# Optimization experiments

Measured on AMD Instinct MI355X. Metric: run time of the kernel, lower is better.

## Reference

```python
import math
import jax, jax.numpy as jnp
import numpy as np

B, HRV, WRV, CRV = 1, 32, 512, 64
CBEV, HB, WB = 128, 256, 256
D, COUT, K, HEADS, P = 128, 128, 5, 8, 6
HD = D // HEADS
NBINS = 110
RMAX, BIN = 55.0, 0.5
XMIN, XMAX, YMIN, YMAX = -55.0, 55.0, -55.0, 55.0

_ELEV = np.array([-30.67, -29.33, -28.0, -26.66, -25.33, -24.0, -22.67, -21.33,
                  -20.0, -18.67, -17.33, -16.0, -14.67, -13.33, -12.0, -10.67,
                  -9.33, -8.0, -6.66, -5.33, -4.0, -2.67, -1.33, 0.0, 1.33,
                  2.67, 4.0, 5.33, 6.67, 8.0, 9.33, 10.67], dtype=np.float32)

def _make_uvec():
    az_line = np.linspace(-math.pi, math.pi, WRV + 1, dtype=np.float32)[:-1]
    az = az_line + 0.5 * (az_line[1] - az_line[0])
    elev = np.deg2rad(_ELEV[::-1].reshape(HRV, -1).mean(axis=1)).astype(np.float32)
    az2 = np.broadcast_to(az[None, :], (HRV, WRV))
    el2 = np.broadcast_to(elev[:, None], (HRV, WRV))
    ux = np.cos(az2) * np.cos(el2)
    uy = np.sin(az2) * np.cos(el2)
    uz = np.broadcast_to(np.sin(el2), (HRV, WRV))
    return jnp.asarray(ux), jnp.asarray(uy), jnp.asarray(uz)

_UX, _UY, _UZ = _make_uvec()

def _lin(x, w, b):
    # 1x1 conv / Linear: w is torch-layout [Cout, Cin]
    return jnp.einsum('...c,oc->...o', x, w) + b

def _gn(x, gamma, beta, groups, eps=1e-5):
    Bn, H, W, C = x.shape
    xg = x.reshape(Bn, H, W, groups, C // groups)
    mu = xg.mean(axis=(1, 2, 4), keepdims=True)
    var = ((xg - mu) ** 2).mean(axis=(1, 2, 4), keepdims=True)
    xg = (xg - mu) * jax.lax.rsqrt(var + eps)
    return xg.reshape(Bn, H, W, C) * gamma + beta

def _gelu(x):
    return jax.nn.gelu(x, approximate=False)

def _conv3x3_circ(x, w):
    # torch Conv2d(3x3, padding=1, padding_mode='circular', bias=False)
    xp = jnp.pad(x, ((0, 0), (1, 1), (1, 1), (0, 0)), mode='wrap')
    k = jnp.transpose(w, (2, 3, 1, 0))  # OIHW -> HWIO
    return jax.lax.conv_general_dilated(xp, k, (1, 1), 'VALID',
                                        dimension_numbers=('NHWC', 'HWIO', 'NHWC'))

def _deform_sample(v, loc, aw):
    # v: [B, HB*WB, HEADS, HD]; loc: [B,Nq,HEADS,P,2] normalized; aw: [B,Nq,HEADS,P]
    # Emulates grid_sample(bilinear, zeros padding, align_corners=False).
    Bq = v.shape[0]
    vflat = jnp.transpose(v, (0, 2, 1, 3))       # [B, H, HW, hd]
    loc_t = jnp.transpose(loc, (0, 2, 1, 3, 4))  # [B, H, Nq, P, 2]
    aw_t = jnp.transpose(aw, (0, 2, 1, 3))       # [B, H, Nq, P]
    x = loc_t[..., 0] * WB - 0.5
    y = loc_t[..., 1] * HB - 0.5
    x0 = jnp.floor(x); y0 = jnp.floor(y)
    wx1 = x - x0; wy1 = y - y0
    x0i = x0.astype(jnp.int32); y0i = y0.astype(jnp.int32)
    gather = jax.vmap(jax.vmap(lambda vf, idx: vf[idx]))  # over B, heads
    def corner(xi, yi, wgt, acc):
        valid = (xi >= 0) & (xi < WB) & (yi >= 0) & (yi < HB)
        idx = jnp.clip(yi, 0, HB - 1) * WB + jnp.clip(xi, 0, WB - 1)
        g = gather(vflat, idx)  # [B, H, Nq, P, hd]
        return acc + g * (wgt * valid.astype(g.dtype))[..., None]
    acc = jnp.zeros(x.shape + (HD,), dtype=v.dtype)
    acc = corner(x0i,     y0i,     (1 - wx1) * (1 - wy1), acc)
    acc = corner(x0i + 1, y0i,     wx1 * (1 - wy1), acc)
    acc = corner(x0i,     y0i + 1, (1 - wx1) * wy1, acc)
    acc = corner(x0i + 1, y0i + 1, wx1 * wy1, acc)
    out = (acc * aw_t[..., None]).sum(axis=3)    # [B, H, Nq, hd]
    return jnp.transpose(out, (0, 2, 1, 3)).reshape(Bq, -1, D)

def _forward(x_rv, bev, lidar2ego_mat, wq, bq, wv, bv, wo, bo,
             qd_w1, qd_b1, qd_w2, qd_b2,
             rh_w1, rh_b1, rh_g1, rh_be1, rh_w2, rh_g2, rh_be2, rh_w3, rh_b3,
             off_w, off_b, aw_w, aw_b, vp_w, vp_b, op_w, op_b):
    Bq = x_rv.shape[0]
    Q0 = _lin(x_rv, wq, bq)                                   # [B,Hrv,Wrv,D]
    Vmap = _lin(jnp.transpose(bev, (0, 2, 3, 1)), wv, bv)     # [B,HB,WB,D]
    uvec = jnp.broadcast_to(jnp.stack([_UX, _UY, _UZ], axis=-1)[None], (Bq, HRV, WRV, 3))
    h = _gelu(_gn(_lin(jnp.concatenate([x_rv, uvec], axis=-1), rh_w1, rh_b1), rh_g1, rh_be1, 8))
    h = _gelu(_gn(_conv3x3_circ(h, rh_w2), rh_g2, rh_be2, 8))
    depth_logits = _lin(h, rh_w3, rh_b3)                      # [B,Hrv,Wrv,NBINS]
    depth_dist = jax.nn.softmax(depth_logits, axis=-1)
    topk_prob, topk_idx = jax.lax.top_k(depth_dist, K)        # [B,Hrv,Wrv,K]
    topk_depths = jnp.minimum(BIN * (topk_idx.astype(jnp.float32) + 0.5), RMAX - 0.5 * BIN)
    xl = topk_depths * _UX[None, :, :, None]
    yl = topk_depths * _UY[None, :, :, None]
    zl = topk_depths * _UZ[None, :, :, None]
    p = jnp.stack([xl, yl, zl, jnp.ones_like(xl)], axis=-1)   # [B,Hrv,Wrv,K,4]
    pe = jnp.einsum('bhwki,ij->bhwkj', p, lidar2ego_mat[0])
    rx = (pe[..., 0] - XMIN) / (XMAX - XMIN)
    ry = (pe[..., 1] - YMIN) / (YMAX - YMIN)
    ref_pts = jnp.stack([jnp.clip(rx, 0.0, 1.0), jnp.clip(ry, 0.0, 1.0)], axis=-1).reshape(Bq, -1, 2)
    qin = jnp.concatenate([jnp.broadcast_to(Q0[:, :, :, None, :], (Bq, HRV, WRV, K, D)),
                           (topk_depths / RMAX)[..., None]], axis=-1)
    query = _lin(_gelu(_lin(qin, qd_w1, qd_b1)), qd_w2, qd_b2).reshape(Bq, -1, D)
    value = Vmap.reshape(Bq, -1, D)
    # --- MSDA (mmcv MultiScaleDeformableAttention, 1 level) ---
    v = _lin(value, vp_w, vp_b).reshape(Bq, -1, HEADS, HD)
    Nq = query.shape[1]
    off = _lin(query, off_w, off_b).reshape(Bq, Nq, HEADS, P, 2)
    aw = jax.nn.softmax(_lin(query, aw_w, aw_b).reshape(Bq, Nq, HEADS, P), axis=-1)
    loc = ref_pts[:, :, None, None, :] + off / jnp.array([WB, HB], dtype=jnp.float32)
    y_msda = _lin(_deform_sample(v, loc, aw), op_w, op_b) + query  # residual add
    y_msda = y_msda.reshape(Bq, HRV, WRV, K, D)
    wgt = topk_prob / (topk_prob.sum(axis=-1, keepdims=True) + 1e-8)
    y = (y_msda * wgt[..., None]).sum(axis=3)
    y = _lin(y, wo, bo)                                       # [B,Hrv,Wrv,COUT]
    return y, jnp.transpose(depth_logits, (0, 3, 1, 2))

def setup_inputs():
    key = jax.random.key(0)
    ks = jax.random.split(key, 32)
    def rn(i, shape, s):
        return jax.random.normal(ks[i], shape, dtype=jnp.float32) * s
    return dict(
        x_rv=rn(0, (B, HRV, WRV, CRV), 1.0),
        bev=rn(1, (B, CBEV, HB, WB), 1.0),
        lidar2ego_mat=jnp.eye(4, dtype=jnp.float32)[None] + rn(2, (1, 4, 4), 0.01),
        wq=rn(3, (D, CRV), 0.05), bq=rn(4, (D,), 0.01),
        wv=rn(5, (D, CBEV), 0.05), bv=rn(6, (D,), 0.01),
        wo=rn(7, (COUT, D), 0.05), bo=rn(8, (COUT,), 0.01),
        qd_w1=rn(9, (D, D + 1), 0.05), qd_b1=rn(10, (D,), 0.01),
        qd_w2=rn(11, (D, D), 0.05), qd_b2=rn(12, (D,), 0.01),
        rh_w1=rn(13, (128, CRV + 3), 0.05), rh_b1=rn(14, (128,), 0.01),
        rh_g1=jnp.ones((128,), jnp.float32), rh_be1=jnp.zeros((128,), jnp.float32),
        rh_w2=rn(15, (64, 128, 3, 3), 0.05),
        rh_g2=jnp.ones((64,), jnp.float32), rh_be2=jnp.zeros((64,), jnp.float32),
        rh_w3=rn(16, (NBINS, 64), 0.05), rh_b3=rn(17, (NBINS,), 0.01),
        off_w=rn(18, (HEADS * P * 2, D), 0.02), off_b=rn(19, (HEADS * P * 2,), 2.0),
        aw_w=rn(20, (HEADS * P, D), 0.02), aw_b=rn(21, (HEADS * P,), 0.01),
        vp_w=rn(22, (D, D), 0.05), vp_b=rn(23, (D,), 0.01),
        op_w=rn(24, (D, D), 0.05), op_b=rn(25, (D,), 0.01),
    )

def reference(x_rv, bev, lidar2ego_mat, wq, bq, wv, bv, wo, bo,
              qd_w1, qd_b1, qd_w2, qd_b2,
              rh_w1, rh_b1, rh_g1, rh_be1, rh_w2, rh_g2, rh_be2, rh_w3, rh_b3,
              off_w, off_b, aw_w, aw_b, vp_w, vp_b, op_w, op_b):
    return _forward(x_rv, bev, lidar2ego_mat, wq, bq, wv, bv, wo, bo,
                    qd_w1, qd_b1, qd_w2, qd_b2,
                    rh_w1, rh_b1, rh_g1, rh_be1, rh_w2, rh_g2, rh_be2, rh_w3, rh_b3,
                    off_w, off_b, aw_w, aw_b, vp_w, vp_b, op_w, op_b)
```

## Files before the change

kernel.cpp:

```cpp
#include <hip/hip_runtime.h>
#include <math.h>

#define NT 256

typedef unsigned short u16;
typedef unsigned int u32;
typedef _Float16 f16;
typedef __attribute__((ext_vector_type(2))) unsigned int u32x2;
typedef __attribute__((ext_vector_type(4))) unsigned int u32x4;
typedef __attribute__((ext_vector_type(4))) float f32x4;
typedef __attribute__((ext_vector_type(8))) short s16x8;
typedef __attribute__((ext_vector_type(8))) _Float16 f16x8;

namespace {

__device__ const float c_elev[32] = {
  -30.67f,-29.33f,-28.0f,-26.66f,-25.33f,-24.0f,-22.67f,-21.33f,
  -20.0f,-18.67f,-17.33f,-16.0f,-14.67f,-13.33f,-12.0f,-10.67f,
  -9.33f,-8.0f,-6.66f,-5.33f,-4.0f,-2.67f,-1.33f,0.0f,1.33f,
  2.67f,4.0f,5.33f,6.67f,8.0f,9.33f,10.67f };

__device__ __forceinline__ float gelu_f(float x) {
  return 0.5f * x * (1.0f + erff(x * 0.70710678118654752440f));
}
// ... 15 lines not shown
__device__ __forceinline__ u32 packsplit(float x) {
  f16 h = (f16)x;
  f16 l = (f16)(x - (float)h);
  return (u32)__builtin_bit_cast(u16, h) | ((u32)__builtin_bit_cast(u16, l) << 16);
}
__device__ __forceinline__ void unpack16(u32x4 a, u32x4 b, f16x8& hi, f16x8& lo) {
  u32x4 h, l;
  h[0] = (a[0] & 0xFFFFu) | (a[1] << 16);  l[0] = (a[0] >> 16) | (a[1] & 0xFFFF0000u);
  h[1] = (a[2] & 0xFFFFu) | (a[3] << 16);  l[1] = (a[2] >> 16) | (a[3] & 0xFFFF0000u);
  h[2] = (b[0] & 0xFFFFu) | (b[1] << 16);  l[2] = (b[0] >> 16) | (b[1] & 0xFFFF0000u);
  h[3] = (b[2] & 0xFFFFu) | (b[3] << 16);  l[3] = (b[2] >> 16) | (b[3] & 0xFFFF0000u);
  hi = __builtin_bit_cast(f16x8, h);
  lo = __builtin_bit_cast(f16x8, l);
}

template<int COREAL, int CO, int KPAD, int CI, int PROD, int AMODE, bool DOGELU, bool OBF>
__global__ __launch_bounds__(NT)
void slin(const float* __restrict__ Af, const float* __restrict__ A2,
          const u32* __restrict__ Wp, const float* __restrict__ bias,
          float* __restrict__ outF, u16* __restrict__ outB)
{
  constexpr int BM = 64;
  constexpr int NFR = CO / 16;
  constexpr int KS = KPAD / 32;
  __shared__ u32 lds[BM * KPAD];
  const int tid = threadIdx.x;
  const long row0 = (long)blockIdx.x * BM;

  for (int i = tid; i < BM * (KPAD / 4); i += NT) {
    int r = i / (KPAD / 4), c = (i % (KPAD / 4)) * 4;
    long pix = row0 + r;
    u32x4 o;
    if constexpr (AMODE == 0) {
      if (c + 3 < CI) {
        f32x4 v = *(const f32x4*)(Af + pix * CI + c);
#pragma unroll
        for (int e = 0; e < 4; e++) o[e] = packsplit(v[e]);
      } else {
#pragma unroll
        for (int e = 0; e < 4; e++) {
          int cc = c + e;
          o[e] = packsplit(cc < CI ? Af[pix * CI + cc] : 0.f);
        }
      }
    } else {
      if (c + 3 < 64) {
        f32x4 v = *(const f32x4*)(Af + pix * 64 + c);
#pragma unroll
        for (int e = 0; e < 4; e++) o[e] = packsplit(v[e]);
      } else {
#pragma unroll
        for (int e = 0; e < 4; e++) {
          int cc = c + e;
          float x = (cc < 64) ? Af[pix * 64 + cc] : ((cc < 67) ? A2[pix * 3 + cc - 64] : 0.f);
          o[e] = packsplit(x);
        }
      }
// ... 37 lines not shown
    if (col >= COREAL) continue;
    float bcol = bias[col];
#pragma unroll
    for (int r = 0; r < 4; r++) {
      long row = row0 + mb + kq * 4 + r;
      float val = acc[nf][r] + bcol;
      if constexpr (DOGELU) val = gelu_f(val);
      if constexpr (OBF) outB[row * COREAL + col] = bf16rne(val);
      else               outF[row * COREAL + col] = val;
    }
  }
}

__global__ __launch_bounds__(NT)
void conv_mfma(const float* __restrict__ X, const u32* __restrict__ Wc,
               float* __restrict__ Y)
{
  __shared__ u32 lds[4 * 18 * 128];
  const int tid = threadIdx.x;
  const int bRow = (blockIdx.x >> 5) * 2;
  const int bCol = (blockIdx.x & 31) * 16;

  for (int i = tid; i < 4 * 18 * 32; i += NT) {
    int c4 = (i & 31) * 4;
    int col = (i >> 5) % 18;
    int row = i / (18 * 32);
    int gy = (bRow + row - 1 + 32) & 31;
    int gx = (bCol + col - 1 + 512) & 511;
    f32x4 v = *(const f32x4*)(X + ((long)gy * 512 + gx) * 128 + c4);
    u32x4 o;
#pragma unroll
    for (int e = 0; e < 4; e++) o[e] = packsplit(v[e]);
    *(u32x4*)((char*)lds + ((((row * 18 + col) * 128 + c4) * 4) ^ ((col & 7) << 4))) = o;
  }
  __syncthreads();

  const int wave = tid >> 6, lane = tid & 63;
  const int wm = wave >> 1;
  const int nb = (wave & 1) * 32;
  const int lr = lane & 15, kq = lane >> 4;

  f32x4 acc[2] = {};
  for (int t = 0; t < 9; t++) {
    const int ky = t / 3, kx = t % 3;
    const int wrow = wm + ky;
    const int wcol = lr + kx;
    const u32 sw = (wcol & 7) << 4;
// ... 120 lines not shown
        if constexpr (DEPTH) val += ew * (A2[row] * (1.0f / 55.0f));
        if constexpr (DOGELU) val = gelu_f(val);
        if constexpr (SPLIT) {
          if (col < 96) outF[row * 96 + col] = val;
          else if (col < 144) outB[row * 48 + (col - 96)] = bf16rne(val);
        } else {
          if constexpr (WF) outF[row * CO + col] = val;
          if constexpr (WBF) outB[row * CO + col] = bf16rne(val);
        }
      }
    }
  }
}

__global__ __launch_bounds__(NT)
void final_gemm(const u16* __restrict__ A, const u16* __restrict__ Wc,
                const float* __restrict__ cvec, float* __restrict__ outY)
{
  __shared__ char As[64 * 512];
  const int tid = threadIdx.x;
  const long row0 = (long)blockIdx.x * 64;
  for (int i = tid; i < 64 * 32; i += NT) {
    int r = i >> 5, ck = i & 31;
    u32x4 v = ((const u32x4*)(A + (row0 + r) * 256))[ck];
    *(u32x4*)(As + ((r * 512 + ck * 16) ^ ((r & 7) << 4))) = v;
  }
  __syncthreads();
  const int wave = tid >> 6, lane = tid & 63;
  const int mb = wave * 16;
  const int lr = lane & 15, kq = lane >> 4;
  f32x4 acc[8] = {};
#pragma unroll
  for (int ks = 0; ks < 8; ks++) {
    const int kof = (ks * 32 + kq * 8) * 2;
    const int r = mb + lr;
    s16x8 af = *(const s16x8*)(As + ((r * 512 + kof) ^ ((r & 7) << 4)));
#pragma unroll
    for (int nf = 0; nf < 8; nf++) {
      s16x8 bfr = *(const s16x8*)(Wc + (nf * 16 + lr) * 256 + ks * 32 + kq * 8);
      acc[nf] = __builtin_amdgcn_mfma_f32_16x16x32_bf16(af, bfr, acc[nf], 0, 0, 0);
    }
  }
#pragma unroll
  for (int nf = 0; nf < 8; nf++) {
    int col = nf * 16 + lr;
    float bcol = cvec[col];
#pragma unroll
    for (int r = 0; r < 4; r++) {
      long row = row0 + mb + kq * 4 + r;
      outY[row * 128 + col] = acc[nf][r] + bcol;
    }
  }
}

__global__ __launch_bounds__(NT)
void combine_kernel(const u16* __restrict__ smp, const u16* __restrict__ query,
                    const float* __restrict__ wgt, u16* __restrict__ acat)
{
  const long idx = (long)blockIdx.x * NT + threadIdx.x;
  const long pix = idx >> 3;
  const int c0 = (idx & 7) * 16;
  float w[5];
#pragma unroll
  for (int k = 0; k < 5; k++) w[k] = wgt[pix * 5 + k];
  float as[16] = {}, aq[16] = {};
#pragma unroll
  for (int k = 0; k < 5; k++) {
    const u32x4* sp = (const u32x4*)(smp + (pix * 5 + k) * 128 + c0);
    const u32x4* qp = (const u32x4*)(query + (pix * 5 + k) * 128 + c0);
    u32x4 s0 = sp[0], s1 = sp[1], q0 = qp[0], q1 = qp[1];
#pragma unroll
    for (int e = 0; e < 4; e++) {
      as[2 * e]     += w[k] * bflo(s0[e]);  as[2 * e + 1] += w[k] * bfhi(s0[e]);
      as[8 + 2 * e] += w[k] * bflo(s1[e]);  as[9 + 2 * e] += w[k] * bfhi(s1[e]);
      aq[2 * e]     += w[k] * bflo(q0[e]);  aq[2 * e + 1] += w[k] * bfhi(q0[e]);
      aq[8 + 2 * e] += w[k] * bflo(q1[e]);  aq[9 + 2 * e] += w[k] * bfhi(q1[e]);
    }
  }
  u32x4 o0, o1, o2, o3;
#pragma unroll
  for (int e = 0; e < 4; e++) {
    o0[e] = (u32)bf16rne(as[2 * e]) | ((u32)bf16rne(as[2 * e + 1]) << 16);
    o1[e] = (u32)bf16rne(as[8 + 2 * e]) | ((u32)bf16rne(as[9 + 2 * e]) << 16);
    o2[e] = (u32)bf16rne(aq[2 * e]) | ((u32)bf16rne(aq[2 * e + 1]) << 16);
    o3[e] = (u32)bf16rne(aq[8 + 2 * e]) | ((u32)bf16rne(aq[9 + 2 * e]) << 16);
  }
  u32x4* dst = (u32x4*)(acat + pix * 256 + c0);
  dst[0] = o0; dst[1] = o1;
  u32x4* dst2 = (u32x4*)(acat + pix * 256 + 128 + c0);
  dst2[0] = o2; dst2[1] = o3;
}

__global__ void wcomb_kernel(const float* __restrict__ vp_w, const float* __restrict__ wv,
                             const float* __restrict__ vp_b, const float* __restrict__ bv,
                             u16* __restrict__ wc, float* __restrict__ bc)
{
  int o = blockIdx.x;
  int c = threadIdx.x;
  float s = 0.f;
  for (int m = 0; m < 128; m++) s += vp_w[o * 128 + m] * wv[m * 128 + c];
  wc[o * 128 + c] = bf16rne(s);
  if (c == 0) {
    float b = vp_b[o];
    for (int m = 0; m < 128; m++) b += vp_w[o * 128 + m] * bv[m];
    bc[o] = b;
  }
}

__global__ void wopcomb_kernel(const float* __restrict__ wo, const float* __restrict__ op_w,
                               const float* __restrict__ op_b, const float* __restrict__ bo,
                               u16* __restrict__ Wcat, float* __restrict__ cvec)
{
  int o = blockIdx.x;
  int c = threadIdx.x;
  float s = 0.f;
  for (int m = 0; m < 128; m++) s += wo[o * 128 + m] * op_w[m * 128 + c];
  Wcat[o * 256 + c] = bf16rne(s);
  Wcat[o * 256 + 128 + c] = bf16rne(wo[o * 128 + c]);
  if (c == 0) {
    float b = bo[o];
    for (int m = 0; m < 128; m++) b += wo[o * 128 + m] * op_b[m];
    cvec[o] = b;
  }
}

__global__ void cvtw_kernel(const float* __restrict__ qd_w1, const float* __restrict__ qd_w2,
                            const float* __restrict__ off_w, const float* __restrict__ aw_w,
                            const float* __restrict__ off_b, const float* __restrict__ aw_b,
                            u16* Wq1, u16* Wq2, u16* Wmg, float* mgbias, float* w1last)
{
  int i = blockIdx.x * NT + threadIdx.x;
  if (i < 16384) {
    int r = i >> 7, c = i & 127;
    Wq1[i] = bf16rne(qd_w1[r * 129 + c]);
    Wq2[i] = bf16rne(qd_w2[i]);
  }
  if (i < 20480) {
    int r = i >> 7, c = i & 127;
    float v = (r < 96) ? off_w[r * 128 + c] : ((r < 144) ? aw_w[(r - 96) * 128 + c] : 0.f);
    Wmg[i] = bf16rne(v);
  }
  if (i < 160) mgbias[i] = (i < 96) ? off_b[i] : ((i < 144) ? aw_b[i - 96] : 0.f);
  if (i < 128) w1last[i] = qd_w1[i * 129 + 128];
}

__global__ void packw_kernel(const float* __restrict__ rh_w1, const float* __restrict__ rh_w3,
                             const float* __restrict__ wq, const float* __restrict__ rh_w2,
                             u32* Wh1, u32* Wlog, u32* Wq0, u32* Wcv)
{
  int i = blockIdx.x * NT + threadIdx.x;
  if (i < 128 * 96) {
    int r = i / 96, c = i % 96;
    Wh1[i] = packsplit(c < 67 ? rh_w1[r * 67 + c] : 0.f);
  }
  if (i < 112 * 64) {
    int r = i / 64, c = i % 64;
    Wlog[i] = packsplit(r < 110 ? rh_w3[r * 64 + c] : 0.f);
  }
  if (i < 128 * 64) Wq0[i] = packsplit(wq[i]);
  if (i < 9 * 64 * 128) {
    int t = i / (64 * 128), o = (i / 128) % 64, c = i % 128;
    Wcv[i] = packsplit(rh_w2[(o * 128 + c) * 9 + t]);
  }
}

__global__ void uvec_kernel(float* __restrict__ uvec)
{
  int pix = blockIdx.x * NT + threadIdx.x;
  if (pix >= 16384) return;
  int hr = pix >> 9;
  int w = pix & 511;
  float el = c_elev[31 - hr] * 0.017453292519943295f;
  float az = -3.14159265358979323846f + ((float)w + 0.5f) * (6.283185307179586477f / 512.0f);
  float ce = cosf(el);
  uvec[pix * 3 + 0] = cosf(az) * ce;
  uvec[pix * 3 + 1] = sinf(az) * ce;
  uvec[pix * 3 + 2] = sinf(el);
}

template<int C, int S>
__global__ __launch_bounds__(NT)
void gn_stats_kernel(const float* __restrict__ X, int Npix, float* __restrict__ gs)
{
  constexpr int PPB = NT / C;
  int tid = threadIdx.x;
  int c = tid % C;
  int psub = tid / C;
  float sum = 0.f, ss = 0.f;
  for (long pix = (long)blockIdx.x * PPB + psub; pix < Npix; pix += (long)gridDim.x * PPB) {
    float v = X[pix * C + c];
    sum += v; ss += v * v;
  }
  __shared__ float ls[8][2];
  if (tid < 16) ls[tid / 2][tid % 2] = 0.f;
  __syncthreads();
  int g = c / S;
  atomicAdd(&ls[g][0], sum);
  atomicAdd(&ls[g][1], ss);
  __syncthreads();
  if (tid < 16) atomicAdd(&gs[tid], ls[tid / 2][tid % 2]);
}

template<int C, int S>
__global__ void gn_apply_kernel(float* __restrict__ X, long total, int Npix,
                                const float* __restrict__ gs,
                                const float* __restrict__ gamma, const float* __restrict__ beta)
{
  float cnt = (float)Npix * (float)S;
  for (long i = (long)blockIdx.x * NT + threadIdx.x; i < total; i += (long)gridDim.x * NT) {
    int c = (int)(i % C);
    int g = c / S;
    float mu = gs[g * 2] / cnt;
    float var = gs[g * 2 + 1] / cnt - mu * mu;
    float v = (X[i] - mu) * rsqrtf(var + 1e-5f);
    v = v * gamma[c] + beta[c];
    X[i] = gelu_f(v);
  }
}

__global__ __launch_bounds__(NT)
void tlogits_kernel(const float* __restrict__ logits, float* __restrict__ out1)
{
  __shared__ float ls[128][111];
  int p0 = blockIdx.x * 128;
  for (int i = threadIdx.x; i < 128 * 110; i += NT) {
    int p = i / 110, c = i % 110;
    ls[p][c] = logits[(long)(p0 + p) * 110 + c];
  }
  __syncthreads();
  for (int i = threadIdx.x; i < 110 * 128; i += NT) {
    int c = i / 128, p = i % 128;
    out1[(long)c * 16384 + p0 + p] = ls[p][c];
  }
}
// ... 27 lines not shown
    pr[j] = expf(bv - m) / den;
    pi[j] = bi;
    if (bi == lane) v0 = -1e30f;
    if (bi == lane + 64) v1 = -1e30f;
  }
  if (lane == 0) {
    float tot = pr[0] + pr[1] + pr[2] + pr[3] + pr[4] + 1e-8f;
#pragma unroll
    for (int j = 0; j < 5; j++) {
      depths[pix * 5 + j] = fminf(0.5f * ((float)pi[j] + 0.5f), 54.75f);
      wgt[pix * 5 + j] = pr[j] / tot;
    }
  }
}

__global__ void refq_kernel(const float* __restrict__ depths, const float* __restrict__ uvec,
                            const float* __restrict__ L44, float* __restrict__ refq)
{
  long q = (long)blockIdx.x * NT + threadIdx.x;
  if (q >= 81920) return;
  long pix = q / 5;
  float d = depths[q];
  float px = d * uvec[pix * 3 + 0];
  float py = d * uvec[pix * 3 + 1];
  float pz = d * uvec[pix * 3 + 2];
  float pex = px * L44[0] + py * L44[4] + pz * L44[8] + L44[12];
  float pey = px * L44[1] + py * L44[5] + pz * L44[9] + L44[13];
  float rx = (pex + 55.0f) / 110.0f;
  float ry = (pey + 55.0f) / 110.0f;
  refq[q * 2 + 0] = fminf(fmaxf(rx, 0.f), 1.f);
  refq[q * 2 + 1] = fminf(fmaxf(ry, 0.f), 1.f);
}

__global__ __launch_bounds__(NT)
void msda_kernel(const u16* __restrict__ V, const float* __restrict__ refq,
                 const float* __restrict__ offb, const u16* __restrict__ awb,
                 u16* __restrict__ S)
{
  const int tid = threadIdx.x;
  const int kk = blockIdx.x >> 9;
  const int pg = blockIdx.x & 511;
  const long pix = (long)pg * 32 + (tid >> 3);
  const int h = tid & 7;
  const long q = pix * 5 + kk;
  const int c0 = h * 16;
  const float rx = refq[q * 2 + 0], ry = refq[q * 2 + 1];

  const u32* ap32 = (const u32*)(awb + q * 48 + h * 6);
  u32 aw0 = ap32[0], aw1 = ap32[1], aw2 = ap32[2];
  float a[6] = { bflo(aw0), bfhi(aw0), bflo(aw1), bfhi(aw1), bflo(aw2), bfhi(aw2) };
  float mx = fmaxf(fmaxf(fmaxf(a[0], a[1]), fmaxf(a[2], a[3])), fmaxf(a[4], a[5]));
  float se = 0.f;
#pragma unroll
  for (int p = 0; p < 6; p++) { a[p] = __expf(a[p] - mx); se += a[p]; }
  const float inv = 1.0f / se;

  const f32x4* opv = (const f32x4*)(offb + q * 96 + h * 12);
  f32x4 of0 = opv[0], of1 = opv[1], of2 = opv[2];
  const float ox[6] = { of0[0], of0[2], of1[0], of1[2], of2[0], of2[2] };
  const float oy[6] = { of0[1], of0[3], of1[1], of1[3], of2[1], of2[3] };

  float acc[16];
#pragma unroll
  for (int j = 0; j < 16; j++) acc[j] = 0.f;

#pragma unroll
  for (int p = 0; p < 6; p++) {
    float x = (rx + ox[p] * (1.0f / 256.0f)) * 256.0f - 0.5f;
    float y = (ry + oy[p] * (1.0f / 256.0f)) * 256.0f - 0.5f;
    float x0f = floorf(x), y0f = floorf(y);
    float wx = x - x0f, wy = y - y0f;
    int ix = (int)x0f, iy = (int)y0f;
    float awp = a[p] * inv;
    float wx0 = ((unsigned)ix < 256u) ? (1.f - wx) : 0.f;
    float wx1 = ((unsigned)(ix + 1) < 256u) ? wx : 0.f;
    float wy0 = ((unsigned)iy < 256u) ? (awp * (1.f - wy)) : 0.f;
    float wy1 = ((unsigned)(iy + 1) < 256u) ? (awp * wy) : 0.f;
    int xc0 = min(max(ix, 0), 255), xc1 = min(max(ix + 1, 0), 255);
    int yc0 = min(max(iy, 0), 255), yc1 = min(max(iy + 1, 0), 255);
#pragma unroll
    for (int cy = 0; cy < 2; cy++) {
      int yc = cy ? yc1 : yc0;
      float wyv = cy ? wy1 : wy0;
#pragma unroll
      for (int cx = 0; cx < 2; cx++) {
        int xc = cx ? xc1 : xc0;
        float m = (cx ? wx1 : wx0) * wyv;
        const u32x4* vp = (const u32x4*)(V + (yc * 256 + xc) * 128 + c0);
        u32x4 v0 = vp[0], v1 = vp[1];
#pragma unroll
        for (int e = 0; e < 4; e++) {
          acc[2 * e]     += m * bflo(v0[e]);  acc[2 * e + 1] += m * bfhi(v0[e]);
          acc[8 + 2 * e] += m * bflo(v1[e]);  acc[9 + 2 * e] += m * bfhi(v1[e]);
        }
      }
    }
  }
  u32x4 o0, o1;
#pragma unroll
  for (int e = 0; e < 4; e++) {
    o0[e] = (u32)bf16rne(acc[2 * e]) | ((u32)bf16rne(acc[2 * e + 1]) << 16);
    o1[e] = (u32)bf16rne(acc[8 + 2 * e]) | ((u32)bf16rne(acc[9 + 2 * e]) << 16);
  }
  u32x4* dst = (u32x4*)(S + q * 128 + c0);
  dst[0] = o0; dst[1] = o1;
}

}

extern "C" void kernel_launch(void* const* d_in, const int* in_sizes, int n_in,
                              void* d_out, int out_size, void* d_ws, size_t ws_size,
                              hipStream_t stream)
{
  (void)in_sizes; (void)n_in; (void)out_size; (void)ws_size;
  const float* x_rv   = (const float*)d_in[0];
  const float* bev    = (const float*)d_in[1];
  const float* L44    = (const float*)d_in[2];
  const float* wq     = (const float*)d_in[3];
  const float* bq     = (const float*)d_in[4];
  const float* wv     = (const float*)d_in[5];
// ... 27 lines not shown

  char* wsb = (char*)d_ws;
  size_t off = 0;
  auto alloc = [&](size_t bytes) -> char* {
    char* p = wsb + off;
    off += (bytes + 255) & ~(size_t)255;
    return p;
  };

  u16*   wcomb  = (u16*)alloc(32768);
  float* bcomb  = (float*)alloc(512);
  float* uvec   = (float*)alloc(196608);
  float* stats  = (float*)alloc(128);
  float* depths = (float*)alloc(327680);
  float* wgtb   = (float*)alloc(327680);
  float* refqb  = (float*)alloc(655360);
  float* w1last = (float*)alloc(512);
  u16*   Wq1    = (u16*)alloc(32768);
  u16*   Wq2    = (u16*)alloc(32768);
  u16*   Wmg    = (u16*)alloc(40960);
  float* mgbias = (float*)alloc(640);
  u16*   Wcat   = (u16*)alloc(65536);
  float* cvec   = (float*)alloc(512);
  u32*   Wh1    = (u32*)alloc(49152);
  u32*   Wlog   = (u32*)alloc(28672);
  u32*   Wq0    = (u32*)alloc(32768);
  u32*   Wcv    = (u32*)alloc(294912);
  char*  S1     = alloc(20971520);
  char*  S2     = alloc(4194304);
  char*  S3     = alloc(16777216);
  char*  S4     = alloc(20971520);
  char*  S5     = alloc(20971520);
  float* offbuf = (float*)alloc(31457280);
  u16*   awbf   = (u16*)alloc(7864320);

  float* h1buf  = (float*)S1;
  float* logits = (float*)(S1 + 8388608);
  float* h2buf  = (float*)(S1 + 15597568);
  u16*   smp    = (u16*)S1;
  u16*   Q0bf   = (u16*)S2;
  u16*   vbuf   = (u16*)S3;
  u16*   q1bf   = (u16*)S4;
  u16*   acat   = (u16*)S4;
  u16*   querybf= (u16*)S5;

  float* stats1 = stats;
  float* stats2 = stats + 16;

  hipMemsetAsync((void*)stats, 0, 128, stream);

  wcomb_kernel<<<128, 128, 0, stream>>>(vp_w, wv, vp_b, bv, wcomb, bcomb);
  wopcomb_kernel<<<128, 128, 0, stream>>>(woW, op_w, op_b, boB, Wcat, cvec);
  uvec_kernel<<<64, NT, 0, stream>>>(uvec);
  cvtw_kernel<<<80, NT, 0, stream>>>(qd_w1, qd_w2, off_w, aw_w, off_b, aw_b,
                                     Wq1, Wq2, Wmg, mgbias, w1last);
  packw_kernel<<<288, NT, 0, stream>>>(rh_w1, rh_w3, wq, rh_w2, Wh1, Wlog, Wq0, Wcv);

  slin<128, 128, 64, 64, 1, 0, false, true><<<256, NT, 0, stream>>>(
      x_rv, nullptr, Wq0, bq, nullptr, Q0bf);

  slin<128, 128, 96, 67, 3, 1, false, false><<<256, NT, 0, stream>>>(
      x_rv, uvec, Wh1, rh_b1, h1buf, nullptr);
  gn_stats_kernel<128, 16><<<512, NT, 0, stream>>>(h1buf, 16384, stats1);
  gn_apply_kernel<128, 16><<<2048, NT, 0, stream>>>(h1buf, 16384L * 128, 16384, stats1, rh_g1, rh_be1);
  conv_mfma<<<512, NT, 0, stream>>>(h1buf, Wcv, h2buf);
  gn_stats_kernel<64, 8><<<512, NT, 0, stream>>>(h2buf, 16384, stats2);
  gn_apply_kernel<64, 8><<<1024, NT, 0, stream>>>(h2buf, 16384L * 64, 16384, stats2, rh_g2, rh_be2);
  slin<110, 112, 64, 64, 3, 0, false, false><<<256, NT, 0, stream>>>(
      h2buf, nullptr, Wlog, rh_b3, logits, nullptr);
  tlogits_kernel<<<128, NT, 0, stream>>>(logits, outL);
  topk_kernel<<<4096, NT, 0, stream>>>(logits, depths, wgtb);
  refq_kernel<<<320, NT, 0, stream>>>(depths, uvec, L44, refqb);

  mfma_lin<128, 4, false, false, false, true, false><<<1024, NT, 0, stream>>>(
      bev, nullptr, wcomb, bcomb, nullptr, nullptr, vbuf, 65536);

  mfma_lin<128, 1, true, true, false, true, false><<<1280, NT, 0, stream>>>(
      Q0bf, depths, Wq1, qd_b1, w1last, nullptr, q1bf, 0);
  mfma_lin<128, 0, false, false, false, true, false><<<1280, NT, 0, stream>>>(
      q1bf, nullptr, Wq2, qd_b2, nullptr, nullptr, querybf, 0);

  mfma_lin<160, 0, false, false, false, false, true><<<1280, NT, 0, stream>>>(
      querybf, nullptr, Wmg, mgbias, nullptr, offbuf, awbf, 0);

  msda_kernel<<<2560, NT, 0, stream>>>(vbuf, refqb, offbuf, awbf, smp);

  combine_kernel<<<512, NT, 0, stream>>>(smp, querybf, wgtb, acat);

  final_gemm<<<256, NT, 0, stream>>>(acat, Wcat, cvec, outY);
}
```

Measured before the change: 452.3 us.

## Fuse GroupNorm apply, query MLP, combine/outproj, refq, and merge prep kernels

New measurement: 406.9 us. -10.0%, faster.

```diff
diff --git a/kernel.cpp b/kernel.cpp
--- a/kernel.cpp
+++ b/kernel.cpp
@@ -53,10 +53,12 @@
   lo = __builtin_bit_cast(f16x8, l);
 }
 
-template<int COREAL, int CO, int KPAD, int CI, int PROD, int AMODE, bool DOGELU, bool OBF>
+template<int COREAL, int CO, int KPAD, int CI, int PROD, int AMODE, bool DOGELU, bool OBF, bool GN = false>
 __global__ __launch_bounds__(NT)
 void slin(const float* __restrict__ Af, const float* __restrict__ A2,
           const u32* __restrict__ Wp, const float* __restrict__ bias,
+          const float* __restrict__ gs, const float* __restrict__ gamma,
+          const float* __restrict__ beta,
           float* __restrict__ outF, u16* __restrict__ outB)
 {
   constexpr int BM = 64;
@@ -74,12 +76,32 @@
       if (c + 3 < CI) {
         f32x4 v = *(const f32x4*)(Af + pix * CI + c);
 #pragma unroll
-        for (int e = 0; e < 4; e++) o[e] = packsplit(v[e]);
+        for (int e = 0; e < 4; e++) {
+          float x = v[e];
+          if constexpr (GN) {
+            int cc = c + e, g = cc >> 3;
+            float mu = gs[2 * g] * (1.0f / 131072.0f);
+            float var = gs[2 * g + 1] * (1.0f / 131072.0f) - mu * mu;
+            x = (x - mu) * rsqrtf(var + 1e-5f) * gamma[cc] + beta[cc];
+            x = gelu_f(x);
+          }
+          o[e] = packsplit(x);
+        }
       } else {
 #pragma unroll
         for (int e = 0; e < 4; e++) {
           int cc = c + e;
-          o[e] = packsplit(cc < CI ? Af[pix * CI + cc] : 0.f);
+          float x = (cc < CI) ? Af[pix * CI + cc] : 0.f;
+          if constexpr (GN) {
+            if (cc < CI) {
+              int g = cc >> 3;
+              float mu = gs[2 * g] * (1.0f / 131072.0f);
+              float var = gs[2 * g + 1] * (1.0f / 131072.0f) - mu * mu;
+              x = (x - mu) * rsqrtf(var + 1e-5f) * gamma[cc] + beta[cc];
+              x = gelu_f(x);
+            }
+          }
+          o[e] = packsplit(x);
         }
       }
     } else {
@@ -147,7 +169,8 @@
 
 __global__ __launch_bounds__(NT)
 void conv_mfma(const float* __restrict__ X, const u32* __restrict__ Wc,
-               float* __restrict__ Y)
+               const float* __restrict__ gs, const float* __restrict__ gamma,
+               const float* __restrict__ beta, float* __restrict__ Y)
 {
   __shared__ u32 lds[4 * 18 * 128];
   const int tid = threadIdx.x;
@@ -163,7 +186,13 @@
     f32x4 v = *(const f32x4*)(X + ((long)gy * 512 + gx) * 128 + c4);
     u32x4 o;
 #pragma unroll
-    for (int e = 0; e < 4; e++) o[e] = packsplit(v[e]);
+    for (int e = 0; e < 4; e++) {
+      int cc = c4 + e, g = cc >> 4;
+      float mu = gs[2 * g] * (1.0f / 262144.0f);
+      float var = gs[2 * g + 1] * (1.0f / 262144.0f) - mu * mu;
+      float x = (v[e] - mu) * rsqrtf(var + 1e-5f) * gamma[cc] + beta[cc];
+      o[e] = packsplit(gelu_f(x));
+    }
     *(u32x4*)((char*)lds + ((((row * 18 + col) * 128 + c4) * 4) ^ ((col & 7) << 4))) = o;
   }
   __syncthreads();
@@ -314,120 +343,230 @@
 }
 
 __global__ __launch_bounds__(NT)
-void final_gemm(const u16* __restrict__ A, const u16* __restrict__ Wc,
-                const float* __restrict__ cvec, float* __restrict__ outY)
+void qmlp_kernel(const u16* __restrict__ Q0, const float* __restrict__ depths,
+                 const u16* __restrict__ W1, const float* __restrict__ b1,
+                 const float* __restrict__ w1last,
+                 const u16* __restrict__ W2, const float* __restrict__ b2,
+                 u16* __restrict__ query)
+{
+  __shared__ char smem[49152];
+  char* As = smem;
+  char* Bs = smem + 16384;
+  const int tid = threadIdx.x;
+  const long row0 = (long)blockIdx.x * 64;
+
+  for (int i = tid; i < 128 * 16; i += NT) {
+    int r = i >> 4, ck = i & 15;
+    u32x4 v = ((const u32x4*)(W1 + r * 128))[ck];
+    *(u32x4*)(Bs + ((r * 256 + ck * 16) ^ ((r & 7) << 4))) = v;
+  }
+  for (int i = tid; i < 64 * 16; i += NT) {
+    int r = i >> 4, ck = i & 15;
+    long src = (row0 + r) / 5;
+    u32x4 v = ((const u32x4*)(Q0 + src * 128))[ck];
+    *(u32x4*)(As + ((r * 256 + ck * 16) ^ ((r & 7) << 4))) = v;
+  }
+  __syncthreads();
+
+  const int wave = tid >> 6, lane = tid & 63;
+  const int wm = wave >> 1, wn = wave & 1;
+  const int mb = wm * 32, nb = wn * 64;
+  const int lr = lane & 15, kq = lane >> 4;
+
+  f32x4 acc[2][4] = {};
+#pragma unroll
+  for (int ks = 0; ks < 4; ks++) {
+    const int kof = (ks * 32 + kq * 8) * 2;
+    s16x8 af[2], bfr[4];
+#pragma unroll
+    for (int mf = 0; mf < 2; mf++) {
+      int r = mb + mf * 16 + lr;
+      af[mf] = *(const s16x8*)(As + ((r * 256 + kof) ^ ((r & 7) << 4)));
+    }
+#pragma unroll
+    for (int nf = 0; nf < 4; nf++) {
+      int r = nb + nf * 16 + lr;
+      bfr[nf] = *(const s16x8*)(Bs + ((r * 256 + kof) ^ ((r & 7) << 4)));
+    }
+#pragma unroll
+    for (int mf = 0; mf < 2; mf++)
+#pragma unroll
+      for (int nf = 0; nf < 4; nf++)
+        acc[mf][nf] = __builtin_amdgcn_mfma_f32_16x16x32_bf16(af[mf], bfr[nf], acc[mf][nf], 0, 0, 0);
+  }
+  __syncthreads();
+
+#pragma unroll
+  for (int mf = 0; mf < 2; mf++) {
+#pragma unroll
+    for (int nf = 0; nf < 4; nf++) {
+      int col = nb + nf * 16 + lr;
+      float bcol = b1[col], ew = w1last[col];
+#pragma unroll
+      for (int r = 0; r < 4; r++) {
+        int lrow = mb + mf * 16 + kq * 4 + r;
+        float val = acc[mf][nf][r] + bcol + ew * (depths[row0 + lrow] * (1.0f / 55.0f));
+        val = gelu_f(val);
+        *(u16*)(As + ((lrow * 256 + col * 2) ^ ((lrow & 7) << 4))) = bf16rne(val);
+      }
+    }
+  }
+  for (int i = tid; i < 128 * 16; i += NT) {
+    int r = i >> 4, ck = i & 15;
+    u32x4 v = ((const u32x4*)(W2 + r * 128))[ck];
+    *(u32x4*)(Bs + ((r * 256 + ck * 16) ^ ((r & 7) << 4))) = v;
+  }
+  __syncthreads();
+
+  f32x4 acc2[2][4] = {};
+#pragma unroll
+  for (int ks = 0; ks < 4; ks++) {
+    const int kof = (ks * 32 + kq * 8) * 2;
+    s16x8 af[2], bfr[4];
+#pragma unroll
+    for (int mf = 0; mf < 2; mf++) {
+      int r = mb + mf * 16 + lr;
+      af[mf] = *(const s16x8*)(As + ((r * 256 + kof) ^ ((r & 7) << 4)));
+    }
+#pragma unroll
+    for (int nf = 0; nf < 4; nf++) {
+      int r = nb + nf * 16 + lr;
+      bfr[nf] = *(const s16x8*)(Bs + ((r * 256 + kof) ^ ((r & 7) << 4)));
+    }
+#pragma unroll
+    for (int mf = 0; mf < 2; mf++)
+#pragma unroll
+      for (int nf = 0; nf < 4; nf++)
+        acc2[mf][nf] = __builtin_amdgcn_mfma_f32_16x16x32_bf16(af[mf], bfr[nf], acc2[mf][nf], 0, 0, 0);
+  }
+#pragma unroll
+  for (int mf = 0; mf < 2; mf++) {
+#pragma unroll
+    for (int nf = 0; nf < 4; nf++) {
+      int col = nb + nf * 16 + lr;
+      float bcol = b2[col];
+#pragma unroll
+      for (int r = 0; r < 4; r++) {
+        long row = row0 + mb + mf * 16 + kq * 4 + r;
+        query[row * 128 + col] = bf16rne(acc2[mf][nf][r] + bcol);
+      }
+    }
+  }
+}
+
+__global__ __launch_bounds__(NT)
+void outproj_kernel(const u16* __restrict__ smp, const u16* __restrict__ query,
+                    const float* __restrict__ wgt, const u16* __restrict__ Wcat,
+                    const float* __restrict__ cvec, float* __restrict__ outY)
 {
   __shared__ char As[64 * 512];
   const int tid = threadIdx.x;
-  const long row0 = (long)blockIdx.x * 64;
-  for (int i = tid; i < 64 * 32; i += NT) {
-    int r = i >> 5, ck = i & 31;
-    u32x4 v = ((const u32x4*)(A + (row0 + r) * 256))[ck];
-    *(u32x4*)(As + ((r * 512 + ck * 16) ^ ((r & 7) << 4))) = v;
-  }
-  __syncthreads();
+  const long pix0 = (long)blockIdx.x * 64;
+
+#pragma unroll
+  for (int t = 0; t < 8; t++) {
+    int task = tid + t * 256;
+    int r = task >> 5, ch = task & 31;
+    long pix = pix0 + r;
+    const u16* src = (ch < 16) ? smp : query;
+    int cc = (ch & 15) * 8;
+    float acc[8] = {};
+#pragma unroll
+    for (int k = 0; k < 5; k++) {
+      float w = wgt[pix * 5 + k];
+      u32x4 v = *(const u32x4*)(src + (pix * 5 + k) * 128 + cc);
+#pragma unroll
+      for (int e = 0; e < 4; e++) {
+        acc[2 * e]     += w * bflo(v[e]);
+        acc[2 * e + 1] += w * bfhi(v[e]);
+      }
+    }
+    u32x4 o;
+#pragma unroll
+    for (int e = 0; e < 4; e++)
+      o[e] = (u32)bf16rne(acc[2 * e]) | ((u32)bf16rne(acc[2 * e + 1]) << 16);
+    *(u32x4*)(As + ((r * 512 + ch * 16) ^ ((r & 7) << 4))) = o;
+  }
+  __syncthreads();
+
   const int wave = tid >> 6, lane = tid & 63;
-  const int mb = wave * 16;
+  const int wm = wave >> 1, wn = wave & 1;
+  const int mb = wm * 32, nb = wn * 64;
   const int lr = lane & 15, kq = lane >> 4;
-  f32x4 acc[8] = {};
+
+  f32x4 acc[2][4] = {};
 #pragma unroll
   for (int ks = 0; ks < 8; ks++) {
     const int kof = (ks * 32 + kq * 8) * 2;
-    const int r = mb + lr;
-    s16x8 af = *(const s16x8*)(As + ((r * 512 + kof) ^ ((r & 7) << 4)));
-#pragma unroll
-    for (int nf = 0; nf < 8; nf++) {
-      s16x8 bfr = *(const s16x8*)(Wc + (nf * 16 + lr) * 256 + ks * 32 + kq * 8);
-      acc[nf] = __builtin_amdgcn_mfma_f32_16x16x32_bf16(af, bfr, acc[nf], 0, 0, 0);
-    }
-  }
-#pragma unroll
-  for (int nf = 0; nf < 8; nf++) {
-    int col = nf * 16 + lr;
-    float bcol = cvec[col];
-#pragma unroll
-    for (int r = 0; r < 4; r++) {
-      long row = row0 + mb + kq * 4 + r;
-      outY[row * 128 + col] = acc[nf][r] + bcol;
-    }
-  }
-}
-
-__global__ __launch_bounds__(NT)
-void combine_kernel(const u16* __restrict__ smp, const u16* __restrict__ query,
-                    const float* __restrict__ wgt, u16* __restrict__ acat)
-{
-  const long idx = (long)blockIdx.x * NT + threadIdx.x;
-  const long pix = idx >> 3;
-  const int c0 = (idx & 7) * 16;
-  float w[5];
-#pragma unroll
-  for (int k = 0; k < 5; k++) w[k] = wgt[pix * 5 + k];
-  float as[16] = {}, aq[16] = {};
-#pragma unroll
-  for (int k = 0; k < 5; k++) {
-    const u32x4* sp = (const u32x4*)(smp + (pix * 5 + k) * 128 + c0);
-    const u32x4* qp = (const u32x4*)(query + (pix * 5 + k) * 128 + c0);
-    u32x4 s0 = sp[0], s1 = sp[1], q0 = qp[0], q1 = qp[1];
-#pragma unroll
-    for (int e = 0; e < 4; e++) {
-      as[2 * e]     += w[k] * bflo(s0[e]);  as[2 * e + 1] += w[k] * bfhi(s0[e]);
-      as[8 + 2 * e] += w[k] * bflo(s1[e]);  as[9 + 2 * e] += w[k] * bfhi(s1[e]);
-      aq[2 * e]     += w[k] * bflo(q0[e]);  aq[2 * e + 1] += w[k] * bfhi(q0[e]);
-      aq[8 + 2 * e] += w[k] * bflo(q1[e]);  aq[9 + 2 * e] += w[k] * bfhi(q1[e]);
-    }
-  }
-  u32x4 o0, o1, o2, o3;
-#pragma unroll
-  for (int e = 0; e < 4; e++) {
-    o0[e] = (u32)bf16rne(as[2 * e]) | ((u32)bf16rne(as[2 * e + 1]) << 16);
-    o1[e] = (u32)bf16rne(as[8 + 2 * e]) | ((u32)bf16rne(as[9 + 2 * e]) << 16);
-    o2[e] = (u32)bf16rne(aq[2 * e]) | ((u32)bf16rne(aq[2 * e + 1]) << 16);
-    o3[e] = (u32)bf16rne(aq[8 + 2 * e]) | ((u32)bf16rne(aq[9 + 2 * e]) << 16);
-  }
-  u32x4* dst = (u32x4*)(acat + pix * 256 + c0);
-  dst[0] = o0; dst[1] = o1;
-  u32x4* dst2 = (u32x4*)(acat + pix * 256 + 128 + c0);
-  dst2[0] = o2; dst2[1] = o3;
-}
-
-__global__ void wcomb_kernel(const float* __restrict__ vp_w, const float* __restrict__ wv,
-                             const float* __restrict__ vp_b, const float* __restrict__ bv,
-                             u16* __restrict__ wc, float* __restrict__ bc)
-{
-  int o = blockIdx.x;
-  int c = threadIdx.x;
-  float s = 0.f;
-  for (int m = 0; m < 128; m++) s += vp_w[o * 128 + m] * wv[m * 128 + c];
-  wc[o * 128 + c] = bf16rne(s);
-  if (c == 0) {
-    float b = vp_b[o];
-    for (int m = 0; m < 128; m++) b += vp_w[o * 128 + m] * bv[m];
-    bc[o] = b;
-  }
-}
-
-__global__ void wopcomb_kernel(const float* __restrict__ wo, const float* __restrict__ op_w,
-                               const float* __restrict__ op_b, const float* __restrict__ bo,
-                               u16* __restrict__ Wcat, float* __restrict__ cvec)
-{
-  int o = blockIdx.x;
-  int c = threadIdx.x;
-  float s = 0.f;
-  for (int m = 0; m < 128; m++) s += wo[o * 128 + m] * op_w[m * 128 + c];
-  Wcat[o * 256 + c] = bf16rne(s);
-  Wcat[o * 256 + 128 + c] = bf16rne(wo[o * 128 + c]);
-  if (c == 0) {
-    float b = bo[o];
-    for (int m = 0; m < 128; m++) b += wo[o * 128 + m] * op_b[m];
-    cvec[o] = b;
-  }
-}
-
-__global__ void cvtw_kernel(const float* __restrict__ qd_w1, const float* __restrict__ qd_w2,
-                            const float* __restrict__ off_w, const float* __restrict__ aw_w,
-                            const float* __restrict__ off_b, const float* __restrict__ aw_b,
-                            u16* Wq1, u16* Wq2, u16* Wmg, float* mgbias, float* w1last)
+    s16x8 af[2], bfr[4];
+#pragma unroll
+    for (int mf = 0; mf < 2; mf++) {
+      int r = mb + mf * 16 + lr;
+      af[mf] = *(const s16x8*)(As + ((r * 512 + kof) ^ ((r & 7) << 4)));
+    }
+#pragma unroll
+    for (int nf = 0; nf < 4; nf++)
+      bfr[nf] = *(const s16x8*)(Wcat + (nb + nf * 16 + lr) * 256 + ks * 32 + kq * 8);
+#pragma unroll
+    for (int mf = 0; mf < 2; mf++)
+#pragma unroll
+      for (int nf = 0; nf < 4; nf++)
+        acc[mf][nf] = __builtin_amdgcn_mfma_f32_16x16x32_bf16(af[mf], bfr[nf], acc[mf][nf], 0, 0, 0);
+  }
+#pragma unroll
+  for (int mf = 0; mf < 2; mf++) {
+#pragma unroll
+    for (int nf = 0; nf < 4; nf++) {
+      int col = nb + nf * 16 + lr;
+      float bcol = cvec[col];
+#pragma unroll
+      for (int r = 0; r < 4; r++) {
+        long row = pix0 + mb + mf * 16 + kq * 4 + r;
+        outY[row * 128 + col] = acc[mf][nf][r] + bcol;
+      }
+    }
+  }
+}
+
+__global__ void prepmm_kernel(const float* __restrict__ vp_w, const float* __restrict__ wv,
+                              const float* __restrict__ vp_b, const float* __restrict__ bv,
+                              const float* __restrict__ wo, const float* __restrict__ op_w,
+                              const float* __restrict__ op_b, const float* __restrict__ bo,
+                              u16* __restrict__ wc, float* __restrict__ bc,
+                              u16* __restrict__ Wcat, float* __restrict__ cvec)
+{
+  int b = blockIdx.x, c = threadIdx.x;
+  if (b < 128) {
+    int o = b;
+    float s = 0.f;
+    for (int m = 0; m < 128; m++) s += vp_w[o * 128 + m] * wv[m * 128 + c];
+    wc[o * 128 + c] = bf16rne(s);
+    if (c == 0) {
+      float bb = vp_b[o];
+      for (int m = 0; m < 128; m++) bb += vp_w[o * 128 + m] * bv[m];
+      bc[o] = bb;
+    }
+  } else {
+    int o = b - 128;
+    float s = 0.f;
+    for (int m = 0; m < 128; m++) s += wo[o * 128 + m] * op_w[m * 128 + c];
+    Wcat[o * 256 + c] = bf16rne(s);
+    Wcat[o * 256 + 128 + c] = bf16rne(wo[o * 128 + c]);
+    if (c == 0) {
+      float bb = bo[o];
+      for (int m = 0; m < 128; m++) bb += wo[o * 128 + m] * op_b[m];
+      cvec[o] = bb;
+    }
+  }
+}
+
+__global__ void prepcvt_kernel(const float* __restrict__ qd_w1, const float* __restrict__ qd_w2,
+                               const float* __restrict__ off_w, const float* __restrict__ aw_w,
+                               const float* __restrict__ off_b, const float* __restrict__ aw_b,
+                               const float* __restrict__ rh_w1, const float* __restrict__ rh_w3,
+                               const float* __restrict__ wq, const float* __restrict__ rh_w2,
+                               u16* Wq1, u16* Wq2, u16* Wmg, float* mgbias, float* w1last,
+                               u32* Wh1, u32* Wlog, u32* Wq0, u32* Wcv, float* uvec)
 {
   int i = blockIdx.x * NT + threadIdx.x;
   if (i < 16384) {
@@ -442,13 +581,6 @@
   }
   if (i < 160) mgbias[i] = (i < 96) ? off_b[i] : ((i < 144) ? aw_b[i - 96] : 0.f);
   if (i < 128) w1last[i] = qd_w1[i * 129 + 128];
-}
-
-__global__ void packw_kernel(const float* __restrict__ rh_w1, const float* __restrict__ rh_w3,
-                             const float* __restrict__ wq, const float* __restrict__ rh_w2,
-                             u32* Wh1, u32* Wlog, u32* Wq0, u32* Wcv)
-{
-  int i = blockIdx.x * NT + threadIdx.x;
   if (i < 128 * 96) {
     int r = i / 96, c = i % 96;
     Wh1[i] = packsplit(c < 67 ? rh_w1[r * 67 + c] : 0.f);
@@ -462,20 +594,15 @@
     int t = i / (64 * 128), o = (i / 128) % 64, c = i % 128;
     Wcv[i] = packsplit(rh_w2[(o * 128 + c) * 9 + t]);
   }
-}
-
-__global__ void uvec_kernel(float* __restrict__ uvec)
-{
-  int pix = blockIdx.x * NT + threadIdx.x;
-  if (pix >= 16384) return;
-  int hr = pix >> 9;
-  int w = pix & 511;
-  float el = c_elev[31 - hr] * 0.017453292519943295f;
-  float az = -3.14159265358979323846f + ((float)w + 0.5f) * (6.283185307179586477f / 512.0f);
-  float ce = cosf(el);
-  uvec[pix * 3 + 0] = cosf(az) * ce;
-  uvec[pix * 3 + 1] = sinf(az) * ce;
-  uvec[pix * 3 + 2] = sinf(el);
+  if (i < 16384) {
+    int hr = i >> 9, w = i & 511;
+    float el = c_elev[31 - hr] * 0.017453292519943295f;
+    float az = -3.14159265358979323846f + ((float)w + 0.5f) * (6.283185307179586477f / 512.0f);
+    float ce = cosf(el);
+    uvec[i * 3 + 0] = cosf(az) * ce;
+    uvec[i * 3 + 1] = sinf(az) * ce;
+    uvec[i * 3 + 2] = sinf(el);
+  }
 }
 
 template<int C, int S>
@@ -501,23 +628,6 @@
   if (tid < 16) atomicAdd(&gs[tid], ls[tid / 2][tid % 2]);
 }
 
-template<int C, int S>
-__global__ void gn_apply_kernel(float* __restrict__ X, long total, int Npix,
-                                const float* __restrict__ gs,
-                                const float* __restrict__ gamma, const float* __restrict__ beta)
-{
-  float cnt = (float)Npix * (float)S;
-  for (long i = (long)blockIdx.x * NT + threadIdx.x; i < total; i += (long)gridDim.x * NT) {
-    int c = (int)(i % C);
-    int g = c / S;
-    float mu = gs[g * 2] / cnt;
-    float var = gs[g * 2 + 1] / cnt - mu * mu;
-    float v = (X[i] - mu) * rsqrtf(var + 1e-5f);
-    v = v * gamma[c] + beta[c];
-    X[i] = gelu_f(v);
-  }
-}
-
 __global__ __launch_bounds__(NT)
 void tlogits_kernel(const float* __restrict__ logits, float* __restrict__ out1)
 {
@@ -575,37 +685,29 @@
   }
 }
 
-__global__ void refq_kernel(const float* __restrict__ depths, const float* __restrict__ uvec,
-                            const float* __restrict__ L44, float* __restrict__ refq)
-{
-  long q = (long)blockIdx.x * NT + threadIdx.x;
-  if (q >= 81920) return;
-  long pix = q / 5;
+__global__ __launch_bounds__(NT)
+void msda_kernel(const u16* __restrict__ V, const float* __restrict__ depths,
+                 const float* __restrict__ uvec, const float* __restrict__ L44,
+                 const float* __restrict__ offb, const u16* __restrict__ awb,
+                 u16* __restrict__ S)
+{
+  const int tid = threadIdx.x;
+  const int kk = blockIdx.x >> 10;
+  const int pg = blockIdx.x & 1023;
+  const long pix = (long)pg * 16 + (tid >> 4);
+  const int h = (tid >> 1) & 7;
+  const int c0 = h * 16 + (tid & 1) * 8;
+  const long q = pix * 5 + kk;
+
   float d = depths[q];
-  float px = d * uvec[pix * 3 + 0];
-  float py = d * uvec[pix * 3 + 1];
-  float pz = d * uvec[pix * 3 + 2];
+  float ux = uvec[pix * 3 + 0], uy = uvec[pix * 3 + 1], uz = uvec[pix * 3 + 2];
+  float px = d * ux, py = d * uy, pz = d * uz;
   float pex = px * L44[0] + py * L44[4] + pz * L44[8] + L44[12];
   float pey = px * L44[1] + py * L44[5] + pz * L44[9] + L44[13];
-  float rx = (pex + 55.0f) / 110.0f;
-  float ry = (pey + 55.0f) / 110.0f;
-  refq[q * 2 + 0] = fminf(fmaxf(rx, 0.f), 1.f);
-  refq[q * 2 + 1] = fminf(fmaxf(ry, 0.f), 1.f);
-}
-
-__global__ __launch_bounds__(NT)
-void msda_kernel(const u16* __restrict__ V, const float* __restrict__ refq,
-                 const float* __restrict__ offb, const u16* __restrict__ awb,
-                 u16* __restrict__ S)
-{
-  const int tid = threadIdx.x;
-  const int kk = blockIdx.x >> 9;
-  const int pg = blockIdx.x & 511;
-  const long pix = (long)pg * 32 + (tid >> 3);
-  const int h = tid & 7;
-  const long q = pix * 5 + kk;
-  const int c0 = h * 16;
-  const float rx = refq[q * 2 + 0], ry = refq[q * 2 + 1];
+  float rx = fminf(fmaxf((pex + 55.0f) * (1.0f / 110.0f), 0.f), 1.f);
+  float ry = fminf(fmaxf((pey + 55.0f) * (1.0f / 110.0f), 0.f), 1.f);
+  float rxs = rx * 256.0f - 0.5f;
+  float rys = ry * 256.0f - 0.5f;
 
   const u32* ap32 = (const u32*)(awb + q * 48 + h * 6);
   u32 aw0 = ap32[0], aw1 = ap32[1], aw2 = ap32[2];
@@ -621,14 +723,14 @@
   const float ox[6] = { of0[0], of0[2], of1[0], of1[2], of2[0], of2[2] };
   const float oy[6] = { of0[1], of0[3], of1[1], of1[3], of2[1], of2[3] };
 
-  float acc[16];
-#pragma unroll
-  for (int j = 0; j < 16; j++) acc[j] = 0.f;
+  float acc[8];
+#pragma unroll
+  for (int j = 0; j < 8; j++) acc[j] = 0.f;
 
 #pragma unroll
   for (int p = 0; p < 6; p++) {
-    float x = (rx + ox[p] * (1.0f / 256.0f)) * 256.0f - 0.5f;
-    float y = (ry + oy[p] * (1.0f / 256.0f)) * 256.0f - 0.5f;
+    float x = rxs + ox[p];
+    float y = rys + oy[p];
     float x0f = floorf(x), y0f = floorf(y);
     float wx = x - x0f, wy = y - y0f;
     int ix = (int)x0f, iy = (int)y0f;
@@ -641,30 +743,26 @@
     int yc0 = min(max(iy, 0), 255), yc1 = min(max(iy + 1, 0), 255);
 #pragma unroll
     for (int cy = 0; cy < 2; cy++) {
-      int yc = cy ? yc1 : yc0;
+      int yb = (cy ? yc1 : yc0) << 15;
       float wyv = cy ? wy1 : wy0;
 #pragma unroll
       for (int cx = 0; cx < 2; cx++) {
-        int xc = cx ? xc1 : xc0;
+        int idx = yb + ((cx ? xc1 : xc0) << 7) + c0;
         float m = (cx ? wx1 : wx0) * wyv;
-        const u32x4* vp = (const u32x4*)(V + (yc * 256 + xc) * 128 + c0);
-        u32x4 v0 = vp[0], v1 = vp[1];
+        u32x4 v = *(const u32x4*)(V + idx);
 #pragma unroll
         for (int e = 0; e < 4; e++) {
-          acc[2 * e]     += m * bflo(v0[e]);  acc[2 * e + 1] += m * bfhi(v0[e]);
-          acc[8 + 2 * e] += m * bflo(v1[e]);  acc[9 + 2 * e] += m * bfhi(v1[e]);
+          acc[2 * e]     += m * bflo(v[e]);
+          acc[2 * e + 1] += m * bfhi(v[e]);
         }
       }
     }
   }
-  u32x4 o0, o1;
-#pragma unroll
-  for (int e = 0; e < 4; e++) {
-    o0[e] = (u32)bf16rne(acc[2 * e]) | ((u32)bf16rne(acc[2 * e + 1]) << 16);
-    o1[e] = (u32)bf16rne(acc[8 + 2 * e]) | ((u32)bf16rne(acc[9 + 2 * e]) << 16);
-  }
-  u32x4* dst = (u32x4*)(S + q * 128 + c0);
-  dst[0] = o0; dst[1] = o1;
+  u32x4 o;
+#pragma unroll
+  for (int e = 0; e < 4; e++)
+    o[e] = (u32)bf16rne(acc[2 * e]) | ((u32)bf16rne(acc[2 * e + 1]) << 16);
+  *(u32x4*)(S + q * 128 + c0) = o;
 }
 
 }
@@ -722,7 +820,6 @@
   float* stats  = (float*)alloc(128);
   float* depths = (float*)alloc(327680);
   float* wgtb   = (float*)alloc(327680);
-  float* refqb  = (float*)alloc(655360);
   float* w1last = (float*)alloc(512);
   u16*   Wq1    = (u16*)alloc(32768);
   u16*   Wq2    = (u16*)alloc(32768);
@@ -737,7 +834,6 @@
   char*  S1     = alloc(20971520);
   char*  S2     = alloc(4194304);
   char*  S3     = alloc(16777216);
-  char*  S4     = alloc(20971520);
   char*  S5     = alloc(20971520);
   float* offbuf = (float*)alloc(31457280);
   u16*   awbf   = (u16*)alloc(7864320);
@@ -748,8 +844,6 @@
   u16*   smp    = (u16*)S1;
   u16*   Q0bf   = (u16*)S2;
   u16*   vbuf   = (u16*)S3;
-  u16*   q1bf   = (u16*)S4;
-  u16*   acat   = (u16*)S4;
   u16*   querybf= (u16*)S5;
 
   float* stats1 = stats;
@@ -757,43 +851,35 @@
 
   hipMemsetAsync((void*)stats, 0, 128, stream);
 
-  wcomb_kernel<<<128, 128, 0, stream>>>(vp_w, wv, vp_b, bv, wcomb, bcomb);
-  wopcomb_kernel<<<128, 128, 0, stream>>>(woW, op_w, op_b, boB, Wcat, cvec);
-  uvec_kernel<<<64, NT, 0, stream>>>(uvec);
-  cvtw_kernel<<<80, NT, 0, stream>>>(qd_w1, qd_w2, off_w, aw_w, off_b, aw_b,
-                                     Wq1, Wq2, Wmg, mgbias, w1last);
-  packw_kernel<<<288, NT, 0, stream>>>(rh_w1, rh_w3, wq, rh_w2, Wh1, Wlog, Wq0, Wcv);
+  prepmm_kernel<<<256, 128, 0, stream>>>(vp_w, wv, vp_b, bv, woW, op_w, op_b, boB,
+                                         wcomb, bcomb, Wcat, cvec);
+  prepcvt_kernel<<<288, NT, 0, stream>>>(qd_w1, qd_w2, off_w, aw_w, off_b, aw_b,
+                                         rh_w1, rh_w3, wq, rh_w2,
+                                         Wq1, Wq2, Wmg, mgbias, w1last,
+                                         Wh1, Wlog, Wq0, Wcv, uvec);
 
   slin<128, 128, 64, 64, 1, 0, false, true><<<256, NT, 0, stream>>>(
-      x_rv, nullptr, Wq0, bq, nullptr, Q0bf);
+      x_rv, nullptr, Wq0, bq, nullptr, nullptr, nullptr, nullptr, Q0bf);
 
   slin<128, 128, 96, 67, 3, 1, false, false><<<256, NT, 0, stream>>>(
-      x_rv, uvec, Wh1, rh_b1, h1buf, nullptr);
+      x_rv, uvec, Wh1, rh_b1, nullptr, nullptr, nullptr, h1buf, nullptr);
   gn_stats_kernel<128, 16><<<512, NT, 0, stream>>>(h1buf, 16384, stats1);
-  gn_apply_kernel<128, 16><<<2048, NT, 0, stream>>>(h1buf, 16384L * 128, 16384, stats1, rh_g1, rh_be1);
-  conv_mfma<<<512, NT, 0, stream>>>(h1buf, Wcv, h2buf);
+  conv_mfma<<<512, NT, 0, stream>>>(h1buf, Wcv, stats1, rh_g1, rh_be1, h2buf);
   gn_stats_kernel<64, 8><<<512, NT, 0, stream>>>(h2buf, 16384, stats2);
-  gn_apply_kernel<64, 8><<<1024, NT, 0, stream>>>(h2buf, 16384L * 64, 16384, stats2, rh_g2, rh_be2);
-  slin<110, 112, 64, 64, 3, 0, false, false><<<256, NT, 0, stream>>>(
-      h2buf, nullptr, Wlog, rh_b3, logits, nullptr);
+  slin<110, 112, 64, 64, 3, 0, false, false, true><<<256, NT, 0, stream>>>(
+      h2buf, nullptr, Wlog, rh_b3, stats2, rh_g2, rh_be2, logits, nullptr);
   tlogits_kernel<<<128, NT, 0, stream>>>(logits, outL);
   topk_kernel<<<4096, NT, 0, stream>>>(logits, depths, wgtb);
-  refq_kernel<<<320, NT, 0, stream>>>(depths, uvec, L44, refqb);
 
   mfma_lin<128, 4, false, false, false, true, false><<<1024, NT, 0, stream>>>(
       bev, nullptr, wcomb, bcomb, nullptr, nullptr, vbuf, 65536);
 
-  mfma_lin<128, 1, true, true, false, true, false><<<1280, NT, 0, stream>>>(
-      Q0bf, depths, Wq1, qd_b1, w1last, nullptr, q1bf, 0);
-  mfma_lin<128, 0, false, false, false, true, false><<<1280, NT, 0, stream>>>(
-      q1bf, nullptr, Wq2, qd_b2, nullptr, nullptr, querybf, 0);
+  qmlp_kernel<<<1280, NT, 0, stream>>>(Q0bf, depths, Wq1, qd_b1, w1last, Wq2, qd_b2, querybf);
 
   mfma_lin<160, 0, false, false, false, false, true><<<1280, NT, 0, stream>>>(
       querybf, nullptr, Wmg, mgbias, nullptr, offbuf, awbf, 0);
 
-  msda_kernel<<<2560, NT, 0, stream>>>(vbuf, refqb, offbuf, awbf, smp);
-
-  combine_kernel<<<512, NT, 0, stream>>>(smp, querybf, wgtb, acat);
-
-  final_gemm<<<256, NT, 0, stream>>>(acat, Wcat, cvec, outY);
-}
+  msda_kernel<<<5120, NT, 0, stream>>>(vbuf, depths, uvec, L44, offbuf, awbf, smp);
+
+  outproj_kernel<<<256, NT, 0, stream>>>(smp, querybf, wgtb, Wcat, cvec, outY);
+}
```
